# Performance work log

Measured on AMD Instinct MI355X. Metric: run time of the kernel, lower is better.

Reference implementation:

```python
import jax, jax.numpy as jnp
import numpy as np

KEEPRATE = 0.5


def setup_inputs() -> dict:
    key = jax.random.key(0)
    k1, k2, k3 = jax.random.split(key, 3)
    N, C, T, V, K = 64, 128, 256, 25, 3
    x = jax.random.normal(k1, (N, C, T, V), dtype=jnp.float32)
    A = jax.random.uniform(k2, (N, K, V, V), dtype=jnp.float32)
    p = jax.random.normal(k3, (C * T, 1), dtype=jnp.float32)
    return {"x": x, "A": A, "p": p}


def reference(x, A, p):
    N, C, T, V = x.shape
    Vk = int(KEEPRATE * V)  # number of joints kept
    # [N, V, C*T]
    xr = jnp.transpose(x.reshape(N, C * T, V), (0, 2, 1))
    # l2-normalized projection vector, score per node
    pn = p * jax.lax.rsqrt(jnp.sum(p * p))
    y = xr @ pn                       # [N, V, 1]
    ys = y[..., 0]                    # [N, V]
    idx = jnp.argsort(-ys, axis=-1)[:, :Vk]   # [N, Vk] top-k node indices
    y_hat = jax.nn.sigmoid(jnp.take_along_axis(ys, idx, axis=1))[..., None]  # [N, Vk, 1]
    xg = jnp.take_along_axis(xr, idx[..., None], axis=1) * y_hat             # [N, Vk, C*T]
    # adjacency squaring then row+col gather of kept nodes
    A2 = A @ A                        # [N, K, V, V]

    def _sel(a2, i):                  # a2: [K, V, V], i: [Vk]
        return a2[:, i][:, :, i]      # [K, Vk, Vk]

    A_out = jax.vmap(_sel)(A2, idx)   # [N, K, Vk, Vk]
    x_out = jnp.transpose(xg, (0, 2, 1)).reshape(N, C, T, Vk)
    return x_out, A_out
```

## Files before the change

### kernel.cpp

```cpp
#include <hip/hip_runtime.h>
#include <hip/hip_bf16.h>
#include <math.h>

constexpr int N  = 64;
constexpr int V  = 25;
constexpr int K  = 3;
constexpr int CT = 32768;
constexpr int VK = 12;
constexpr int SPLIT = 32;
constexpr int ROWS  = 256;
constexpr int CHUNK = CT / SPLIT;
constexpr int TILES = CHUNK / ROWS;
constexpr int NBLK_G = N * (CT / ROWS);

typedef float f32x4 __attribute__((ext_vector_type(4)));


__device__ __forceinline__ void gload_lds16(const float* g, float* l) {
    __builtin_amdgcn_global_load_lds(
        (const __attribute__((address_space(1))) void*)g,
        (__attribute__((address_space(3))) void*)l, 16, 0, 0);
}

__device__ __forceinline__ void stage_wave(const float* __restrict__ gsrc, float* ldsbuf,
                                           int wave, int lane) {
    const float* gw = gsrc + (size_t)wave * 1600;
    float* lw = ldsbuf + wave * 1600;
    #pragma unroll
    for (int i = 0; i < 6; ++i)
        gload_lds16(gw + (size_t)(i * 64 + lane) * 4, lw + i * 256);
    if (lane < 16)
        gload_lds16(gw + (size_t)(384 + lane) * 4, lw + 384 * 4);
}

__global__ __launch_bounds__(256) void k_scores(const float* __restrict__ x,
                                                const float* __restrict__ p,
                                                float* __restrict__ partial_t,
                                                float* __restrict__ p2partial) {
    const int n = blockIdx.x / SPLIT;
    const int s = blockIdx.x % SPLIT;
    const int ct0 = s * CHUNK;
    const float* xn = x + (size_t)n * CT * V;
    const int tid = threadIdx.x, wave = tid >> 6, lane = tid & 63;

    __shared__ float lds[2][ROWS * V];

    float pv[TILES];
    #pragma unroll
    for (int t = 0; t < TILES; ++t) pv[t] = p[ct0 + t * ROWS + tid];

    stage_wave(xn + (size_t)(ct0 + 0 * ROWS) * V, lds[0], wave, lane);
    stage_wave(xn + (size_t)(ct0 + 1 * ROWS) * V, lds[1], wave, lane);

    float acc[V];
    #pragma unroll
    for (int v = 0; v < V; ++v) acc[v] = 0.f;
    float psq = 0.f;

    #pragma unroll
    for (int t = 0; t < TILES; ++t) {
        if (t < TILES - 1) asm volatile("s_waitcnt vmcnt(7)" ::: "memory");
        else               asm volatile("s_waitcnt vmcnt(0)" ::: "memory");

        const float pvt = pv[t];
        psq += pvt * pvt;
        const float* row = lds[t & 1] + tid * V;
        #pragma unroll
        for (int v = 0; v < V; ++v) acc[v] += row[v] * pvt;

        if (t + 2 < TILES) {
            asm volatile("s_waitcnt lgkmcnt(0)" ::: "memory");
            stage_wave(xn + (size_t)(ct0 + (t + 2) * ROWS) * V, lds[t & 1], wave, lane);
        }
    }

    #pragma unroll
    for (int v = 0; v < V; ++v) {
        float a = acc[v];
        #pragma unroll
        for (int off = 32; off > 0; off >>= 1) a += __shfl_down(a, off);
        acc[v] = a;
    }
    #pragma unroll
    for (int off = 32; off > 0; off >>= 1) psq += __shfl_down(psq, off);

    __shared__ float red[4][V];
    __shared__ float redp[4];
    if (lane == 0) {
        #pragma unroll
        for (int v = 0; v < V; ++v) red[wave][v] = acc[v];
        redp[wave] = psq;
    }
    __syncthreads();
    if (tid < V) {
        partial_t[((size_t)n * V + tid) * SPLIT + s] =
            red[0][tid] + red[1][tid] + red[2][tid] + red[3][tid];
    }
    if (tid == V && n == 0) {
        p2partial[s] = redp[0] + redp[1] + redp[2] + redp[3];
    }
}

__global__ __launch_bounds__(64) void k_topk(const float* __restrict__ partial_t,
                                             const float* __restrict__ p2partial,
                                             int* __restrict__ idxbuf,
                                             float* __restrict__ yhatbuf) {
    const int n = blockIdx.x, lane = threadIdx.x;
    float s2 = 0.f;
    #pragma unroll
    for (int i = 0; i < SPLIT; ++i) s2 += p2partial[i];

    float my = 0.f;
    if (lane < V) {
        const float4* pb = (const float4*)(partial_t + ((size_t)n * V + lane) * SPLIT);
        #pragma unroll
        for (int i = 0; i < SPLIT / 4; ++i) {
            float4 q = pb[i];
            my += q.x + q.y + q.z + q.w;
        }
    }
    int rank = 0;
    #pragma unroll
    for (int u = 0; u < V; ++u) {
        const float yu = __shfl(my, u);
        if (yu > my || (yu == my && u < lane)) ++rank;
    }
    if (lane < V && rank < VK) {
        idxbuf[n * VK + rank]  = lane;
        yhatbuf[n * VK + rank] = 1.0f / (1.0f + expf(-my * rsqrtf(s2)));
    }
}

__global__ __launch_bounds__(256) void k_gather_aout(const float* __restrict__ x,
                                                     const float* __restrict__ A,
                                                     const int* __restrict__ idxbuf,
                                                     const float* __restrict__ yhatbuf,
                                                     float* __restrict__ xout,
                                                     float* __restrict__ aout) {
    __shared__ float lds[ROWS * V];
    __shared__ int   swidx[4][VK];
    __shared__ float swyh[4][VK];
    const int tid = threadIdx.x, wave = tid >> 6, lane = tid & 63;

    if (blockIdx.x < (unsigned)NBLK_G) {
        const int n  = blockIdx.x >> 7;
        const int r0 = (blockIdx.x & 127) << 8;

        stage_wave(x + ((size_t)n * CT + r0) * V, lds, wave, lane);
        if (lane < VK) {
            swidx[wave][lane] = idxbuf[n * VK + lane];
            swyh[wave][lane]  = yhatbuf[n * VK + lane];
        }
        asm volatile("s_waitcnt vmcnt(0) lgkmcnt(0)" ::: "memory");

        f32x4* dst = (f32x4*)(xout + ((size_t)n * CT + r0) * VK);
        #pragma unroll
        for (int j = 0; j < 3; ++j) {
            const int f   = 192 * wave + 64 * j + lane;
            const int row = f / 3;
            const int c0  = (f % 3) * 4;
            f32x4 o;
            o.x = lds[row * V + swidx[wave][c0 + 0]] * swyh[wave][c0 + 0];
            o.y = lds[row * V + swidx[wave][c0 + 1]] * swyh[wave][c0 + 1];
            o.z = lds[row * V + swidx[wave][c0 + 2]] * swyh[wave][c0 + 2];
            o.w = lds[row * V + swidx[wave][c0 + 3]] * swyh[wave][c0 + 3];
            __builtin_nontemporal_store(o, &dst[f]);
        }
    } else {
        if (wave != 0) return;
        const int b2 = blockIdx.x - NBLK_G;
        const int n  = b2 / K;
        const int k  = b2 % K;
        if (lane < VK) swidx[0][lane] = idxbuf[n * VK + lane];
        const float* Ak = A + ((size_t)n * K + k) * V * V;
        for (int i = lane; i < V * V; i += 64) lds[i] = Ak[i];
        asm volatile("s_waitcnt vmcnt(0) lgkmcnt(0)" ::: "memory");
        for (int o = lane; o < VK * VK; o += 64) {
            const int a  = o / VK, bc = o % VK;
            const int ia = swidx[0][a], ib = swidx[0][bc];
            float ssum = 0.f;
            #pragma unroll
            for (int m = 0; m < V; ++m) ssum += lds[ia * V + m] * lds[m * V + ib];
            __builtin_nontemporal_store(ssum, &aout[((size_t)n * K + k) * VK * VK + o]);
        }
    }
}

extern "C" void kernel_launch(void* const* d_in, const int* in_sizes, int n_in,
                              void* d_out, int out_size, void* d_ws, size_t ws_size,
                              hipStream_t stream) {
    const float* x = (const float*)d_in[0];
    const float* A = (const float*)d_in[1];
    const float* p = (const float*)d_in[2];

    float* xout = (float*)d_out;
    float* aout = xout + (size_t)N * CT * VK;

    char* ws = (char*)d_ws;
    float* partial_t = (float*)(ws);
    float* p2partial = (float*)(ws + 204800);
    float* yhatbuf   = (float*)(ws + 204928);
    int*   idxbuf    = (int*)  (ws + 208000);

    k_scores<<<N * SPLIT, 256, 0, stream>>>(x, p, partial_t, p2partial);
    k_topk<<<N, 64, 0, stream>>>(partial_t, p2partial, idxbuf, yhatbuf);
    k_gather_aout<<<NBLK_G + N * K, 256, 0, stream>>>(x, A, idxbuf, yhatbuf, xout, aout);
}
```

Before: 89.02 us.

## Cache bf16 transposed copy of x in workspace for the gather pass

The score kernel now also writes a bf16, vertex-major copy of x into the workspace, and a new gather kernel reads only the selected vertex rows from that copy instead of re-reading all of x in fp32. The aim is to cut the second full read of x, paying with extra writes in the first pass. The score kernel also loses its double-buffered prefetch and now waits on each tile before computing. Outputs become bf16-rounded, which is a precision loss against the fp32 reference, and the new path only runs if the workspace is large enough.

```diff
diff --git a/kernel.cpp b/kernel.cpp
--- a/kernel.cpp
+++ b/kernel.cpp
@@ -15,6 +15,17 @@
 
 typedef float f32x4 __attribute__((ext_vector_type(4)));
 
+constexpr size_t XC_OFF   = 212992;
+constexpr size_t XC_BYTES = (size_t)N * V * CT * sizeof(ushort);
+
+__device__ __forceinline__ ushort f2bf(float f) {
+    unsigned u = __float_as_uint(f);
+    u += 0x7FFFu + ((u >> 16) & 1u);
+    return (ushort)(u >> 16);
+}
+__device__ __forceinline__ float bf2f(ushort us) {
+    return __uint_as_float((unsigned)us << 16);
+}
 
 __device__ __forceinline__ void gload_lds16(const float* g, float* l) {
     __builtin_amdgcn_global_load_lds(
@@ -33,44 +44,42 @@
         gload_lds16(gw + (size_t)(384 + lane) * 4, lw + 384 * 4);
 }
 
+template <bool WRITE_XC>
 __global__ __launch_bounds__(256) void k_scores(const float* __restrict__ x,
                                                 const float* __restrict__ p,
                                                 float* __restrict__ partial_t,
-                                                float* __restrict__ p2partial) {
+                                                float* __restrict__ p2partial,
+                                                ushort* __restrict__ xc) {
     const int n = blockIdx.x / SPLIT;
     const int s = blockIdx.x % SPLIT;
     const int ct0 = s * CHUNK;
     const float* xn = x + (size_t)n * CT * V;
+    ushort* xcn = xc + (size_t)n * V * CT;
     const int tid = threadIdx.x, wave = tid >> 6, lane = tid & 63;
 
-    __shared__ float lds[2][ROWS * V];
-
-    float pv[TILES];
-    #pragma unroll
-    for (int t = 0; t < TILES; ++t) pv[t] = p[ct0 + t * ROWS + tid];
-
-    stage_wave(xn + (size_t)(ct0 + 0 * ROWS) * V, lds[0], wave, lane);
-    stage_wave(xn + (size_t)(ct0 + 1 * ROWS) * V, lds[1], wave, lane);
+    __shared__ float lds[ROWS * V];
 
     float acc[V];
     #pragma unroll
     for (int v = 0; v < V; ++v) acc[v] = 0.f;
     float psq = 0.f;
 
-    #pragma unroll
-    for (int t = 0; t < TILES; ++t) {
-        if (t < TILES - 1) asm volatile("s_waitcnt vmcnt(7)" ::: "memory");
-        else               asm volatile("s_waitcnt vmcnt(0)" ::: "memory");
-
-        const float pvt = pv[t];
-        psq += pvt * pvt;
-        const float* row = lds[t & 1] + tid * V;
-        #pragma unroll
-        for (int v = 0; v < V; ++v) acc[v] += row[v] * pvt;
-
-        if (t + 2 < TILES) {
-            asm volatile("s_waitcnt lgkmcnt(0)" ::: "memory");
-            stage_wave(xn + (size_t)(ct0 + (t + 2) * ROWS) * V, lds[t & 1], wave, lane);
+    for (int tile = 0; tile < TILES; ++tile) {
+        const int base_ct = ct0 + tile * ROWS;
+        asm volatile("s_waitcnt lgkmcnt(0)" ::: "memory");
+        stage_wave(xn + (size_t)base_ct * V, lds, wave, lane);
+        asm volatile("s_waitcnt vmcnt(0)" ::: "memory");
+
+        const float pv = p[base_ct + tid];
+        psq += pv * pv;
+        const float* row = lds + tid * V;
+        #pragma unroll
+        for (int v = 0; v < V; ++v) acc[v] += row[v] * pv;
+
+        if (WRITE_XC) {
+            #pragma unroll
+            for (int v = 0; v < V; ++v)
+                xcn[(size_t)v * CT + base_ct + tid] = f2bf(row[v]);
         }
     }
 
@@ -128,6 +137,60 @@
     if (lane < V && rank < VK) {
         idxbuf[n * VK + rank]  = lane;
         yhatbuf[n * VK + rank] = 1.0f / (1.0f + expf(-my * rsqrtf(s2)));
+    }
+}
+
+__global__ __launch_bounds__(256) void k_gather_xc(const ushort* __restrict__ xc,
+                                                   const float* __restrict__ A,
+                                                   const int* __restrict__ idxbuf,
+                                                   const float* __restrict__ yhatbuf,
+                                                   float* __restrict__ xout,
+                                                   float* __restrict__ aout) {
+    __shared__ int   sidx[VK];
+    __shared__ float syh[VK];
+    const int tid = threadIdx.x, wave = tid >> 6, lane = tid & 63;
+
+    if (blockIdx.x < (unsigned)NBLK_G) {
+        const int n  = blockIdx.x >> 7;
+        const int r0 = (blockIdx.x & 127) << 8;
+        if (tid < VK) {
+            sidx[tid] = idxbuf[n * VK + tid];
+            syh[tid]  = yhatbuf[n * VK + tid];
+        }
+        __syncthreads();
+
+        const ushort* xcn = xc + (size_t)n * V * CT + r0;
+        f32x4* dst = (f32x4*)(xout + ((size_t)n * CT + r0) * VK);
+        #pragma unroll
+        for (int j = 0; j < 3; ++j) {
+            const int f   = tid + j * 256;
+            const int row = f / 3;
+            const int c0  = (f % 3) * 4;
+            f32x4 o;
+            o.x = bf2f(xcn[(size_t)sidx[c0 + 0] * CT + row]) * syh[c0 + 0];
+            o.y = bf2f(xcn[(size_t)sidx[c0 + 1] * CT + row]) * syh[c0 + 1];
+            o.z = bf2f(xcn[(size_t)sidx[c0 + 2] * CT + row]) * syh[c0 + 2];
+            o.w = bf2f(xcn[(size_t)sidx[c0 + 3] * CT + row]) * syh[c0 + 3];
+            __builtin_nontemporal_store(o, &dst[f]);
+        }
+    } else {
+        if (wave != 0) return;
+        __shared__ float ldsA[V * V];
+        const int b2 = blockIdx.x - NBLK_G;
+        const int n  = b2 / K;
+        const int k  = b2 % K;
+        if (lane < VK) sidx[lane] = idxbuf[n * VK + lane];
+        const float* Ak = A + ((size_t)n * K + k) * V * V;
+        for (int i = lane; i < V * V; i += 64) ldsA[i] = Ak[i];
+        asm volatile("s_waitcnt vmcnt(0) lgkmcnt(0)" ::: "memory");
+        for (int o = lane; o < VK * VK; o += 64) {
+            const int a  = o / VK, bc = o % VK;
+            const int ia = sidx[a], ib = sidx[bc];
+            float ssum = 0.f;
+            #pragma unroll
+            for (int m = 0; m < V; ++m) ssum += ldsA[ia * V + m] * ldsA[m * V + ib];
+            __builtin_nontemporal_store(ssum, &aout[((size_t)n * K + k) * VK * VK + o]);
+        }
     }
 }
 
@@ -145,14 +208,12 @@
     if (blockIdx.x < (unsigned)NBLK_G) {
         const int n  = blockIdx.x >> 7;
         const int r0 = (blockIdx.x & 127) << 8;
-
         stage_wave(x + ((size_t)n * CT + r0) * V, lds, wave, lane);
         if (lane < VK) {
             swidx[wave][lane] = idxbuf[n * VK + lane];
             swyh[wave][lane]  = yhatbuf[n * VK + lane];
         }
         asm volatile("s_waitcnt vmcnt(0) lgkmcnt(0)" ::: "memory");
-
         f32x4* dst = (f32x4*)(xout + ((size_t)n * CT + r0) * VK);
         #pragma unroll
         for (int j = 0; j < 3; ++j) {
@@ -201,8 +262,17 @@
     float* p2partial = (float*)(ws + 204800);
     float* yhatbuf   = (float*)(ws + 204928);
     int*   idxbuf    = (int*)  (ws + 208000);
-
-    k_scores<<<N * SPLIT, 256, 0, stream>>>(x, p, partial_t, p2partial);
-    k_topk<<<N, 64, 0, stream>>>(partial_t, p2partial, idxbuf, yhatbuf);
-    k_gather_aout<<<NBLK_G + N * K, 256, 0, stream>>>(x, A, idxbuf, yhatbuf, xout, aout);
-}
+    ushort* xc       = (ushort*)(ws + XC_OFF);
+
+    const bool use_xc = ws_size >= XC_OFF + XC_BYTES;
+
+    if (use_xc) {
+        k_scores<true><<<N * SPLIT, 256, 0, stream>>>(x, p, partial_t, p2partial, xc);
+        k_topk<<<N, 64, 0, stream>>>(partial_t, p2partial, idxbuf, yhatbuf);
+        k_gather_xc<<<NBLK_G + N * K, 256, 0, stream>>>(xc, A, idxbuf, yhatbuf, xout, aout);
+    } else {
+        k_scores<false><<<N * SPLIT, 256, 0, stream>>>(x, p, partial_t, p2partial, xc);
+        k_topk<<<N, 64, 0, stream>>>(partial_t, p2partial, idxbuf, yhatbuf);
+        k_gather_aout<<<NBLK_G + N * K, 256, 0, stream>>>(x, A, idxbuf, yhatbuf, xout, aout);
+    }
+}
```

New measurement: 101.2 us. 1.14x slower.
